# Optimization experiments

Hardware: AMD Instinct MI355X
Metric: run time of the kernel (lower is better)

Reference implementation:

```python
import jax, jax.numpy as jnp
import numpy as np
import math

NUM_REF = 8
STD = 5.0
B, D = 8192, 512


def setup_inputs() -> dict:
    key = jax.random.key(0)
    k1, k2 = jax.random.split(key)
    Struct = jax.random.normal(k1, (B, D), dtype=jnp.float32)
    Label = jax.random.uniform(k2, (B,), dtype=jnp.float32)
    return {"Struct": Struct, "Label": Label}


def reference(Struct, Label):
    # Pairwise |label_j - label_i| : [B, B]
    res_abs = jnp.abs(Label[None, :] - Label[:, None])
    # Num_ref nearest labels per sample (torch.sort ascending + take first K)
    _, idx = jax.lax.top_k(-res_abs, NUM_REF)          # [B, K]
    Struct_ref = Struct[idx]                            # [B, K, D]
    Label_ref = jax.lax.stop_gradient(Label[idx])       # [B, K] (detached)
    mean = Label[:, None]                               # [B, 1]
    # Gaussian smoothing weights, normalized over the K refs
    w = jnp.exp(-(Label_ref - mean) ** 2 / (2.0 * STD ** 2)) / (
        jnp.sqrt(jnp.asarray(2.0 * math.pi, Struct.dtype)) * STD)
    w = w / jnp.sum(w, axis=1, keepdims=True)           # [B, K]
    Struct_mean = jnp.einsum("bk,bkd->bd", w, Struct_ref)  # [B, D]
    # cosine similarity between Struct and Struct_mean, averaged over batch
    l1 = Struct / (1e-10 + jnp.linalg.norm(Struct, axis=1, keepdims=True))
    l2 = Struct_mean / (1e-10 + jnp.linalg.norm(Struct_mean, axis=1, keepdims=True))
    sim = jnp.mean(jnp.sum(l1 * l2, axis=1))
    return 1.0 - sim
```

## Files before the change

### kernel.cpp

```cpp
#include <hip/hip_runtime.h>
#include <math.h>

#define BN 8192
#define DN 512
#define KN 8
#define WIN 16

typedef unsigned long long u64;
typedef unsigned int u32;

#define OFF_K0    0
#define OFF_K1    65536
#define OFF_PART  131072

__device__ __forceinline__ u32 flip_f32(u32 f) {
  return f ^ (u32)(((int)f >> 31) | 0x80000000);
}
__device__ __forceinline__ float unflip_f32(u32 f) {
  return __uint_as_float((f & 0x80000000u) ? (f ^ 0x80000000u) : ~f);
}

__device__ __forceinline__ u64 shfl_xor_u64(u64 v, int mask) {
  u32 lo = (u32)v, hi = (u32)(v >> 32);
  lo = (u32)__shfl_xor((int)lo, mask, 64);
  hi = (u32)__shfl_xor((int)hi, mask, 64);
  return ((u64)hi << 32) | lo;
}

__device__ __forceinline__ void lds_merge(const u64* in, u64* out, int R, int tid) {
  for (int o = tid; o < 1024; o += 512) {
    int off = o & (2 * R - 1);
    const u64* A = in + (o - off);
    const u64* B = A + R;
    int lo = off > R ? off - R : 0;
    int hi = off < R ? off : R;
    while (lo < hi) {
      int m = (lo + hi) >> 1;
      if (A[m] < B[off - m - 1]) lo = m + 1; else hi = m;
    }
    int a = lo, b = off - lo;
    u64 va = (a < R) ? A[a] : ~0ull;
    u64 vb = (b < R) ? B[b] : ~0ull;
    out[o] = va < vb ? va : vb;
  }
}

__global__ __launch_bounds__(512) void sort1_kernel(const float* __restrict__ L,
                                                    u64* __restrict__ keys) {
  __shared__ u64 bufA[1024];
  __shared__ u64 bufB[1024];
  const int tid  = threadIdx.x;
  const int lane = tid & 63;
  const int wv   = tid >> 6;
  const int base = blockIdx.x * 1024 + wv * 128;

  const int g0 = base + lane, g1 = base + 64 + lane;
  u64 v0 = ((u64)flip_f32(__float_as_uint(L[g0])) << 32) | (u32)g0;
  u64 v1 = ((u64)flip_f32(__float_as_uint(L[g1])) << 32) | (u32)g1;

#pragma unroll
  for (int k = 2; k <= 128; k <<= 1) {
#pragma unroll
    for (int j = 64; j > 0; j >>= 1) {
      if (j >= k) continue;
      if (j == 64) {
        u64 mn = v0 < v1 ? v0 : v1;
        u64 mx = v0 < v1 ? v1 : v0;
        v0 = mn; v1 = mx;
      } else {
        u64 o0 = shfl_xor_u64(v0, j);
        u64 o1 = shfl_xor_u64(v1, j);
        bool lower = (lane & j) == 0;
        bool up0, up1;
        if (k == 128)     { up0 = true;  up1 = true;  }
        else if (k == 64) { up0 = true;  up1 = false; }
        else { bool u = (lane & k) == 0; up0 = u; up1 = u; }
        bool t0 = (up0 == lower), t1 = (up1 == lower);
        v0 = t0 ? (v0 < o0 ? v0 : o0) : (v0 < o0 ? o0 : v0);
        v1 = t1 ? (v1 < o1 ? v1 : o1) : (v1 < o1 ? o1 : v1);
      }
    }
  }

  bufA[wv * 128 + lane]      = v0;
  bufA[wv * 128 + 64 + lane] = v1;
  __syncthreads();
  lds_merge(bufA, bufB, 128, tid); __syncthreads();
  lds_merge(bufB, bufA, 256, tid); __syncthreads();
  lds_merge(bufA, bufB, 512, tid); __syncthreads();

  keys[blockIdx.x * 1024 + tid]       = bufB[tid];
  keys[blockIdx.x * 1024 + 512 + tid] = bufB[512 + tid];
}

template <int RUN>
__global__ __launch_bounds__(256) void merge_pass_kernel(const u64* __restrict__ in,
                                                         u64* __restrict__ outk) {
  const int t = blockIdx.x * 256 + threadIdx.x;
  const int seg = t / (2 * RUN);
  const int o   = t & (2 * RUN - 1);
  const u64* A = in + seg * 2 * RUN;
  const u64* B = A + RUN;

  int lo = (o > RUN) ? (o - RUN) : 0;
  int hi = (o < RUN) ? o : RUN;
  while (lo < hi) {
    int a = (lo + hi) >> 1;
    if (A[a] < B[o - a - 1]) lo = a + 1; else hi = a;
  }
  const int a = lo, b = o - a;
  u64 va = (a < RUN) ? A[a] : ~0ull;
  u64 vb = (b < RUN) ? B[b] : ~0ull;
  outk[t] = (va < vb) ? va : vb;
}

__global__ __launch_bounds__(256) void wmean_cos_kernel(const float* __restrict__ S,
                                                        const u64* __restrict__ keys,
                                                        float* __restrict__ partials) {
  const int tid  = threadIdx.x;
  const int lane = tid & 63;
  const int wv   = tid >> 6;
  const int blk  = blockIdx.x;
  const int xcd  = blk & 7;
  const int span = blk >> 3;
  const int base = xcd * 1024 + span * 4;

  __shared__ u64 win[4 + 2 * WIN];

  if (tid < 4 + 2 * WIN) {
    int q = base - WIN + tid;
    u64 v = ~0ull;
    if (q >= 0 && q < BN) {
      const u64* A = keys;
      const u64* B = keys + 4096;
      int lo = (q > 4096) ? (q - 4096) : 0;
      int hi = (q < 4096) ? q : 4096;
      while (lo < hi) {
        int a = (lo + hi) >> 1;
        if (A[a] < B[q - a - 1]) lo = a + 1; else hi = a;
      }
      int a = lo, b = q - lo;
      u64 va = (a < 4096) ? A[a] : ~0ull;
      u64 vb = (b < 4096) ? B[b] : ~0ull;
      v = (va < vb) ? va : vb;
    }
    win[tid] = v;
  }
  __syncthreads();

  const int rw = wv;
  const u64 ckey = win[rw + WIN];
  const float Lb = unflip_f32((u32)(ckey >> 32));
  const int   b  = (int)(u32)ckey;

  u64 key = ~0ull;
  if (lane <= 2 * WIN) {
    u64 k = win[rw + lane];
    if (k != ~0ull) {
      float lab = unflip_f32((u32)(k >> 32));
      float dist = fabsf(lab - Lb);
      key = ((u64)__float_as_uint(dist) << 32) | (u32)k;
    }
  }
#pragma unroll
  for (int k = 2; k <= 64; k <<= 1) {
#pragma unroll
    for (int j = 32; j > 0; j >>= 1) {
      if (j >= k) continue;
      u64 o = shfl_xor_u64(key, j);
      bool lower = (lane & j) == 0;
      bool up = (k == 64) ? true : ((lane & k) == 0);
      key = (up == lower) ? (key < o ? key : o) : (key < o ? o : key);
    }
  }
  float e = 0.0f;
  if (lane < 8) {
    float d = __uint_as_float((u32)(key >> 32));
    e = expf(-d * d * (1.0f / 50.0f));
  }
  float ssum = e;
  ssum += __shfl_xor(ssum, 1, 64);
  ssum += __shfl_xor(ssum, 2, 64);
  ssum += __shfl_xor(ssum, 4, 64);
  float wn = e / ssum;

  int ix[KN]; float w[KN];
  int myidx = (int)(u32)key;
#pragma unroll
  for (int k = 0; k < KN; k++) {
    ix[k] = __shfl(myidx, k, 64);
    w[k]  = __shfl(wn,    k, 64);
  }

  const float4* Srow = (const float4*)(S + (size_t)b * DN);
  float4 s0 = Srow[lane];
  float4 s1 = Srow[lane + 64];

  float4 m0 = make_float4(0.f, 0.f, 0.f, 0.f);
  float4 m1 = make_float4(0.f, 0.f, 0.f, 0.f);
#pragma unroll
  for (int k = 0; k < KN; k++) {
    const float4* Nrow = (const float4*)(S + (size_t)ix[k] * DN);
    float4 n0 = Nrow[lane];
    float4 n1 = Nrow[lane + 64];
    float wk = w[k];
    m0.x = fmaf(wk, n0.x, m0.x); m0.y = fmaf(wk, n0.y, m0.y);
    m0.z = fmaf(wk, n0.z, m0.z); m0.w = fmaf(wk, n0.w, m0.w);
    m1.x = fmaf(wk, n1.x, m1.x); m1.y = fmaf(wk, n1.y, m1.y);
    m1.z = fmaf(wk, n1.z, m1.z); m1.w = fmaf(wk, n1.w, m1.w);
  }

  float dot = s0.x * m0.x + s0.y * m0.y + s0.z * m0.z + s0.w * m0.w
            + s1.x * m1.x + s1.y * m1.y + s1.z * m1.z + s1.w * m1.w;
  float ns  = s0.x * s0.x + s0.y * s0.y + s0.z * s0.z + s0.w * s0.w
            + s1.x * s1.x + s1.y * s1.y + s1.z * s1.z + s1.w * s1.w;
  float nm  = m0.x * m0.x + m0.y * m0.y + m0.z * m0.z + m0.w * m0.w
            + m1.x * m1.x + m1.y * m1.y + m1.z * m1.z + m1.w * m1.w;

#pragma unroll
  for (int off = 32; off > 0; off >>= 1) {
    dot += __shfl_down(dot, off, 64);
    ns  += __shfl_down(ns,  off, 64);
    nm  += __shfl_down(nm,  off, 64);
  }

  __shared__ float psim[4];
  if (lane == 0) {
    psim[wv] = dot / ((1e-10f + sqrtf(ns)) * (1e-10f + sqrtf(nm)));
  }
  __syncthreads();
  if (tid == 0) {
    partials[blk] = psim[0] + psim[1] + psim[2] + psim[3];
  }
}

__global__ __launch_bounds__(256) void finalize_kernel(const float* __restrict__ partials,
                                                       float* __restrict__ out) {
  const int tid = threadIdx.x;
  float s = 0.0f;
  for (int i = tid; i < 2048; i += 256) s += partials[i];
#pragma unroll
  for (int off = 32; off > 0; off >>= 1) s += __shfl_down(s, off, 64);
  __shared__ float ps[4];
  if ((tid & 63) == 0) ps[tid >> 6] = s;
  __syncthreads();
  if (tid == 0) {
    float tot = ps[0] + ps[1] + ps[2] + ps[3];
    out[0] = 1.0f - tot * (1.0f / (float)BN);
  }
}

extern "C" void kernel_launch(void* const* d_in, const int* in_sizes, int n_in,
                              void* d_out, int out_size, void* d_ws, size_t ws_size,
                              hipStream_t stream) {
  const float* S = (const float*)d_in[0];
  const float* L = (const float*)d_in[1];
  float* out = (float*)d_out;

  char* ws = (char*)d_ws;
  u64*   keys0    = (u64*)  (ws + OFF_K0);
  u64*   keys1    = (u64*)  (ws + OFF_K1);
  float* partials = (float*)(ws + OFF_PART);

  sort1_kernel<<<8, 512, 0, stream>>>(L, keys0);
  merge_pass_kernel<1024><<<32, 256, 0, stream>>>(keys0, keys1);
  merge_pass_kernel<2048><<<32, 256, 0, stream>>>(keys1, keys0);
  wmean_cos_kernel<<<2048, 256, 0, stream>>>(S, keys0, partials);
  finalize_kernel <<<1, 256, 0, stream>>>(partials, out);
}
```

Baseline: 90.87 us.

## Replace bitonic+merge sort pipeline with single-kernel rank sort

Drops the block bitonic sort and the two global merge passes in favour of one rank-sort kernel. Each of 512 blocks loads all 8192 keys into LDS, and each wave counts how many keys are smaller than its 4 keys to place them directly. The windowed-kNN kernel now reads the already-merged keys straight from global memory into lanes instead of doing a merge-path search, which removes two kernel launches. The cost is O(N^2) comparisons and 64KB of LDS per block, and every block reloads the full label array.

New measurement: 80.81 us. 1.12x faster.

```diff
diff --git a/kernel.cpp b/kernel.cpp
--- a/kernel.cpp
+++ b/kernel.cpp
@@ -9,9 +9,8 @@
 typedef unsigned long long u64;
 typedef unsigned int u32;
 
-#define OFF_K0    0
-#define OFF_K1    65536
-#define OFF_PART  131072
+#define OFF_KEYS  0
+#define OFF_PART  65536
 
 __device__ __forceinline__ u32 flip_f32(u32 f) {
   return f ^ (u32)(((int)f >> 31) | 0x80000000);
@@ -26,92 +25,53 @@
   hi = (u32)__shfl_xor((int)hi, mask, 64);
   return ((u64)hi << 32) | lo;
 }
-
-__device__ __forceinline__ void lds_merge(const u64* in, u64* out, int R, int tid) {
-  for (int o = tid; o < 1024; o += 512) {
-    int off = o & (2 * R - 1);
-    const u64* A = in + (o - off);
-    const u64* B = A + R;
-    int lo = off > R ? off - R : 0;
-    int hi = off < R ? off : R;
-    while (lo < hi) {
-      int m = (lo + hi) >> 1;
-      if (A[m] < B[off - m - 1]) lo = m + 1; else hi = m;
-    }
-    int a = lo, b = off - lo;
-    u64 va = (a < R) ? A[a] : ~0ull;
-    u64 vb = (b < R) ? B[b] : ~0ull;
-    out[o] = va < vb ? va : vb;
-  }
-}
-
-__global__ __launch_bounds__(512) void sort1_kernel(const float* __restrict__ L,
-                                                    u64* __restrict__ keys) {
-  __shared__ u64 bufA[1024];
-  __shared__ u64 bufB[1024];
+__device__ __forceinline__ u64 shfl_u64(u64 v, int src) {
+  u32 lo = (u32)v, hi = (u32)(v >> 32);
+  lo = (u32)__shfl((int)lo, src, 64);
+  hi = (u32)__shfl((int)hi, src, 64);
+  return ((u64)hi << 32) | lo;
+}
+
+__global__ __launch_bounds__(256) void ranksort_kernel(const float* __restrict__ L,
+                                                       u64* __restrict__ keys_out) {
+  __shared__ u64 kk[BN];
   const int tid  = threadIdx.x;
   const int lane = tid & 63;
   const int wv   = tid >> 6;
-  const int base = blockIdx.x * 1024 + wv * 128;
-
-  const int g0 = base + lane, g1 = base + 64 + lane;
-  u64 v0 = ((u64)flip_f32(__float_as_uint(L[g0])) << 32) | (u32)g0;
-  u64 v1 = ((u64)flip_f32(__float_as_uint(L[g1])) << 32) | (u32)g1;
-
-#pragma unroll
-  for (int k = 2; k <= 128; k <<= 1) {
-#pragma unroll
-    for (int j = 64; j > 0; j >>= 1) {
-      if (j >= k) continue;
-      if (j == 64) {
-        u64 mn = v0 < v1 ? v0 : v1;
-        u64 mx = v0 < v1 ? v1 : v0;
-        v0 = mn; v1 = mx;
-      } else {
-        u64 o0 = shfl_xor_u64(v0, j);
-        u64 o1 = shfl_xor_u64(v1, j);
-        bool lower = (lane & j) == 0;
-        bool up0, up1;
-        if (k == 128)     { up0 = true;  up1 = true;  }
-        else if (k == 64) { up0 = true;  up1 = false; }
-        else { bool u = (lane & k) == 0; up0 = u; up1 = u; }
-        bool t0 = (up0 == lower), t1 = (up1 == lower);
-        v0 = t0 ? (v0 < o0 ? v0 : o0) : (v0 < o0 ? o0 : v0);
-        v1 = t1 ? (v1 < o1 ? v1 : o1) : (v1 < o1 ? o1 : v1);
-      }
-    }
-  }
-
-  bufA[wv * 128 + lane]      = v0;
-  bufA[wv * 128 + 64 + lane] = v1;
+
+#pragma unroll
+  for (int t = 0; t < BN / 256; t++) {
+    const int i = tid + t * 256;
+    kk[i] = ((u64)flip_f32(__float_as_uint(L[i])) << 32) | (u32)i;
+  }
   __syncthreads();
-  lds_merge(bufA, bufB, 128, tid); __syncthreads();
-  lds_merge(bufB, bufA, 256, tid); __syncthreads();
-  lds_merge(bufA, bufB, 512, tid); __syncthreads();
-
-  keys[blockIdx.x * 1024 + tid]       = bufB[tid];
-  keys[blockIdx.x * 1024 + 512 + tid] = bufB[512 + tid];
-}
-
-template <int RUN>
-__global__ __launch_bounds__(256) void merge_pass_kernel(const u64* __restrict__ in,
-                                                         u64* __restrict__ outk) {
-  const int t = blockIdx.x * 256 + threadIdx.x;
-  const int seg = t / (2 * RUN);
-  const int o   = t & (2 * RUN - 1);
-  const u64* A = in + seg * 2 * RUN;
-  const u64* B = A + RUN;
-
-  int lo = (o > RUN) ? (o - RUN) : 0;
-  int hi = (o < RUN) ? o : RUN;
-  while (lo < hi) {
-    int a = (lo + hi) >> 1;
-    if (A[a] < B[o - a - 1]) lo = a + 1; else hi = a;
-  }
-  const int a = lo, b = o - a;
-  u64 va = (a < RUN) ? A[a] : ~0ull;
-  u64 vb = (b < RUN) ? B[b] : ~0ull;
-  outk[t] = (va < vb) ? va : vb;
+
+  const int wave_g = blockIdx.x * 4 + wv;
+  const int e0 = wave_g * 4;
+  const u64 k0 = kk[e0 + 0];
+  const u64 k1 = kk[e0 + 1];
+  const u64 k2 = kk[e0 + 2];
+  const u64 k3 = kk[e0 + 3];
+
+  int c0 = 0, c1 = 0, c2 = 0, c3 = 0;
+#pragma unroll 4
+  for (int t = lane; t < BN; t += 64) {
+    const u64 v = kk[t];
+    c0 += (v < k0); c1 += (v < k1); c2 += (v < k2); c3 += (v < k3);
+  }
+#pragma unroll
+  for (int off = 1; off < 64; off <<= 1) {
+    c0 += __shfl_xor(c0, off, 64);
+    c1 += __shfl_xor(c1, off, 64);
+    c2 += __shfl_xor(c2, off, 64);
+    c3 += __shfl_xor(c3, off, 64);
+  }
+  if (lane == 0) {
+    keys_out[c0] = k0;
+    keys_out[c1] = k1;
+    keys_out[c2] = k2;
+    keys_out[c3] = k3;
+  }
 }
 
 __global__ __launch_bounds__(256) void wmean_cos_kernel(const float* __restrict__ S,
@@ -123,69 +83,48 @@
   const int blk  = blockIdx.x;
   const int xcd  = blk & 7;
   const int span = blk >> 3;
-  const int base = xcd * 1024 + span * 4;
-
-  __shared__ u64 win[4 + 2 * WIN];
-
-  if (tid < 4 + 2 * WIN) {
-    int q = base - WIN + tid;
-    u64 v = ~0ull;
-    if (q >= 0 && q < BN) {
-      const u64* A = keys;
-      const u64* B = keys + 4096;
-      int lo = (q > 4096) ? (q - 4096) : 0;
-      int hi = (q < 4096) ? q : 4096;
-      while (lo < hi) {
-        int a = (lo + hi) >> 1;
-        if (A[a] < B[q - a - 1]) lo = a + 1; else hi = a;
-      }
-      int a = lo, b = q - lo;
-      u64 va = (a < 4096) ? A[a] : ~0ull;
-      u64 vb = (b < 4096) ? B[b] : ~0ull;
-      v = (va < vb) ? va : vb;
-    }
-    win[tid] = v;
-  }
-  __syncthreads();
-
-  const int rw = wv;
-  const u64 ckey = win[rw + WIN];
+  const int rr   = xcd * 1024 + span * 4 + wv;
+
+  const int q = rr - WIN + lane;
+  const bool inw = (lane <= 2 * WIN) && (q >= 0) && (q < BN);
+  const u64 wk = inw ? keys[q] : ~0ull;
+
+  const u64 ckey = shfl_u64(wk, WIN);
   const float Lb = unflip_f32((u32)(ckey >> 32));
   const int   b  = (int)(u32)ckey;
 
   u64 key = ~0ull;
-  if (lane <= 2 * WIN) {
-    u64 k = win[rw + lane];
-    if (k != ~0ull) {
-      float lab = unflip_f32((u32)(k >> 32));
-      float dist = fabsf(lab - Lb);
-      key = ((u64)__float_as_uint(dist) << 32) | (u32)k;
-    }
-  }
+  if (wk != ~0ull) {
+    const float lab = unflip_f32((u32)(wk >> 32));
+    const float dist = fabsf(lab - Lb);
+    key = ((u64)__float_as_uint(dist) << 32) | (u32)wk;
+  }
+
 #pragma unroll
   for (int k = 2; k <= 64; k <<= 1) {
 #pragma unroll
     for (int j = 32; j > 0; j >>= 1) {
       if (j >= k) continue;
-      u64 o = shfl_xor_u64(key, j);
-      bool lower = (lane & j) == 0;
-      bool up = (k == 64) ? true : ((lane & k) == 0);
+      const u64 o = shfl_xor_u64(key, j);
+      const bool lower = (lane & j) == 0;
+      const bool up = (k == 64) ? true : ((lane & k) == 0);
       key = (up == lower) ? (key < o ? key : o) : (key < o ? o : key);
     }
   }
+
   float e = 0.0f;
   if (lane < 8) {
-    float d = __uint_as_float((u32)(key >> 32));
+    const float d = __uint_as_float((u32)(key >> 32));
     e = expf(-d * d * (1.0f / 50.0f));
   }
   float ssum = e;
   ssum += __shfl_xor(ssum, 1, 64);
   ssum += __shfl_xor(ssum, 2, 64);
   ssum += __shfl_xor(ssum, 4, 64);
-  float wn = e / ssum;
+  const float wn = e / ssum;
 
   int ix[KN]; float w[KN];
-  int myidx = (int)(u32)key;
+  const int myidx = (int)(u32)key;
 #pragma unroll
   for (int k = 0; k < KN; k++) {
     ix[k] = __shfl(myidx, k, 64);
@@ -193,21 +132,21 @@
   }
 
   const float4* Srow = (const float4*)(S + (size_t)b * DN);
-  float4 s0 = Srow[lane];
-  float4 s1 = Srow[lane + 64];
+  const float4 s0 = Srow[lane];
+  const float4 s1 = Srow[lane + 64];
 
   float4 m0 = make_float4(0.f, 0.f, 0.f, 0.f);
   float4 m1 = make_float4(0.f, 0.f, 0.f, 0.f);
 #pragma unroll
   for (int k = 0; k < KN; k++) {
     const float4* Nrow = (const float4*)(S + (size_t)ix[k] * DN);
-    float4 n0 = Nrow[lane];
-    float4 n1 = Nrow[lane + 64];
-    float wk = w[k];
-    m0.x = fmaf(wk, n0.x, m0.x); m0.y = fmaf(wk, n0.y, m0.y);
-    m0.z = fmaf(wk, n0.z, m0.z); m0.w = fmaf(wk, n0.w, m0.w);
-    m1.x = fmaf(wk, n1.x, m1.x); m1.y = fmaf(wk, n1.y, m1.y);
-    m1.z = fmaf(wk, n1.z, m1.z); m1.w = fmaf(wk, n1.w, m1.w);
+    const float4 n0 = Nrow[lane];
+    const float4 n1 = Nrow[lane + 64];
+    const float wk2 = w[k];
+    m0.x = fmaf(wk2, n0.x, m0.x); m0.y = fmaf(wk2, n0.y, m0.y);
+    m0.z = fmaf(wk2, n0.z, m0.z); m0.w = fmaf(wk2, n0.w, m0.w);
+    m1.x = fmaf(wk2, n1.x, m1.x); m1.y = fmaf(wk2, n1.y, m1.y);
+    m1.z = fmaf(wk2, n1.z, m1.z); m1.w = fmaf(wk2, n1.w, m1.w);
   }
 
   float dot = s0.x * m0.x + s0.y * m0.y + s0.z * m0.z + s0.w * m0.w
@@ -245,7 +184,7 @@
   if ((tid & 63) == 0) ps[tid >> 6] = s;
   __syncthreads();
   if (tid == 0) {
-    float tot = ps[0] + ps[1] + ps[2] + ps[3];
+    const float tot = ps[0] + ps[1] + ps[2] + ps[3];
     out[0] = 1.0f - tot * (1.0f / (float)BN);
   }
 }
@@ -258,13 +197,10 @@
   float* out = (float*)d_out;
 
   char* ws = (char*)d_ws;
-  u64*   keys0    = (u64*)  (ws + OFF_K0);
-  u64*   keys1    = (u64*)  (ws + OFF_K1);
+  u64*   keys     = (u64*)  (ws + OFF_KEYS);
   float* partials = (float*)(ws + OFF_PART);
 
-  sort1_kernel<<<8, 512, 0, stream>>>(L, keys0);
-  merge_pass_kernel<1024><<<32, 256, 0, stream>>>(keys0, keys1);
-  merge_pass_kernel<2048><<<32, 256, 0, stream>>>(keys1, keys0);
-  wmean_cos_kernel<<<2048, 256, 0, stream>>>(S, keys0, partials);
+  ranksort_kernel<<<512, 256, 0, stream>>>(L, keys);
+  wmean_cos_kernel<<<2048, 256, 0, stream>>>(S, keys, partials);
   finalize_kernel <<<1, 256, 0, stream>>>(partials, out);
 }
```
